# Kernel optimization log

Measured on AMD Instinct MI355X. Metric: run time of the kernel, lower is better.

Reference implementation:

```python
import jax, jax.numpy as jnp
import numpy as np

HEADS = 8
PATCH = 3
EPS = 1e-6


def conv2d(x, w, b, padding=0, groups=1):
    out = jax.lax.conv_general_dilated(
        x, w, (1, 1), [(padding, padding), (padding, padding)],
        feature_group_count=groups,
        dimension_numbers=("NCHW", "OIHW", "NCHW"))
    return out + b[None, :, None, None]


def unfold(x, p):
    # F.unfold(x, p, padding=(p-1)//2, stride=1) -> [B, C*p*p, H*W]
    B, C, H, W = x.shape
    pad = (p - 1) // 2
    xp = jnp.pad(x, ((0, 0), (0, 0), (pad, pad), (pad, pad)))
    patches = jnp.stack(
        [xp[:, :, i:i + H, j:j + W] for i in range(p) for j in range(p)],
        axis=2)  # [B, C, p*p, H, W] -- channel-major like torch unfold
    return patches.reshape(B, C * p * p, H * W)


def linear_attn(q, k, v):
    # q,k: [B, h, N, Dk]; v: [B, h, N, Dv]; ReLU-feature linear attention
    kv = jnp.einsum("bhnd,bhne->bhde", k, v)          # [B,h,Dk,Dv]
    ksum = jnp.sum(k, axis=2)                          # [B,h,Dk]
    num = jnp.einsum("bhnd,bhde->bhne", q, kv)         # [B,h,N,Dv]
    den = jnp.einsum("bhnd,bhd->bhn", q, ksum)[..., None] + EPS
    return num / den


def attn_block(x, qkv_w, qkv_b, proj_w, proj_b):
    B, C, H, W = x.shape
    qkv = conv2d(x, qkv_w, qkv_b)                      # [B, 3C, H, W]
    q, k, v = jnp.split(qkv, 3, axis=1)
    q = jax.nn.relu(q)
    k = jax.nn.relu(k)
    qp = unfold(q, PATCH)                              # [B, C*p*p, HW]
    kp = unfold(k, PATCH)
    N = H * W
    qh = qp.reshape(B, HEADS, -1, N).transpose(0, 1, 3, 2)  # [B,h,N,Dk]
    kh = kp.reshape(B, HEADS, -1, N).transpose(0, 1, 3, 2)
    vh = v.reshape(B, HEADS, -1, N).transpose(0, 1, 3, 2)   # [B,h,N,Dv]
    o = linear_attn(qh, kh, vh)                        # [B,h,N,Dv]
    o = o.transpose(0, 1, 3, 2).reshape(B, C, H, W)
    return conv2d(o, proj_w, proj_b, padding=1)


def ffn_block(x, w1, b1, dw, db, w2, b2):
    C = x.shape[1]
    h = jax.nn.gelu(conv2d(x, w1, b1), approximate=False)
    h = jax.nn.gelu(conv2d(h, dw, db, padding=1, groups=C), approximate=False)
    return conv2d(h, w2, b2)


def setup_inputs() -> dict:
    key = jax.random.key(0)
    ks = jax.random.split(key, 12)
    C = 64
    B, H, W = 2, 256, 256
    s = 0.05
    return {
        "x": jax.random.normal(ks[0], (B, C, H, W), jnp.float32),
        "qkv_w": jax.random.normal(ks[1], (3 * C, C, 1, 1), jnp.float32) * s,
        "qkv_b": jax.random.normal(ks[2], (3 * C,), jnp.float32) * s,
        "proj_w": jax.random.normal(ks[3], (C, C, 3, 3), jnp.float32) * s,
        "proj_b": jax.random.normal(ks[4], (C,), jnp.float32) * s,
        "ffn1_w": jax.random.normal(ks[5], (C, C, 1, 1), jnp.float32) * s,
        "ffn1_b": jax.random.normal(ks[6], (C,), jnp.float32) * s,
        "dw_w": jax.random.normal(ks[7], (C, 1, 3, 3), jnp.float32) * s,
        "dw_b": jax.random.normal(ks[8], (C,), jnp.float32) * s,
        "ffn2_w": jax.random.normal(ks[9], (C, C, 1, 1), jnp.float32) * s,
        "ffn2_b": jax.random.normal(ks[10], (C,), jnp.float32) * s,
    }


def reference(x, qkv_w, qkv_b, proj_w, proj_b, ffn1_w, ffn1_b, dw_w, dw_b, ffn2_w, ffn2_b):
    x = x + attn_block(x, qkv_w, qkv_b, proj_w, proj_b)
    x = x + ffn_block(x, ffn1_w, ffn1_b, dw_w, dw_b, ffn2_w, ffn2_b)
    return x
```

## Files before the change

### kernel.cpp

```cpp
#include <hip/hip_runtime.h>
#include <hip/hip_bf16.h>

typedef __hip_bfloat16 bf16;
typedef __attribute__((ext_vector_type(8))) short short8;
typedef __attribute__((ext_vector_type(4))) short short4v;
typedef __attribute__((ext_vector_type(4))) float floatx4;

#define NPIX 65536

__device__ __forceinline__ float b2f(bf16 v) { return __bfloat162float(v); }
__device__ __forceinline__ bf16 f2b(float v) { return __float2bfloat16(v); }
__device__ __forceinline__ short f2bs(float v) { bf16 t = __float2bfloat16(v); return *(short*)&t; }
__device__ __forceinline__ float us2f(unsigned short u) {
  union { unsigned int i; float f; } t; t.i = ((unsigned int)u) << 16; return t.f;
}
__device__ __forceinline__ float gelu_f(float v) {
  return 0.5f * v * (1.f + erff(v * 0.7071067811865476f));
}

#define OFF_KV  50331648u
#define OFF_KS  50368512u
#define OFF_WP  50373120u

__global__ void k_zero(float* __restrict__ p, int n) {
  int i = blockIdx.x * 256 + threadIdx.x;
  if (i < n) p[i] = 0.f;
}

__global__ void k_pack(const float* __restrict__ pw, bf16* __restrict__ wpack) {
  int i = blockIdx.x * 256 + threadIdx.x;
  int p = i >> 12, rem = i & 4095;
  int co = rem >> 6, ci = rem & 63;
  wpack[i] = f2b(pw[(co * 64 + ci) * 9 + p]);
}

__device__ __forceinline__ void stage_f32(const float* __restrict__ src, bf16* tile) {
  int tid = threadIdx.x;
  int px = tid & 127, chalf = tid >> 7;
#pragma unroll
  for (int it = 0; it < 8; ++it) {
    int ci0 = it * 8 + chalf * 4;
    short4v w;
#pragma unroll
    for (int j = 0; j < 4; ++j) w[j] = f2bs(src[((size_t)(ci0 + j) << 16) + px]);
    *(short4v*)&tile[px * 72 + ci0] = w;
  }
}

__device__ __forceinline__ void stage_bf16(const bf16* __restrict__ src, bf16* tile) {
  int tid = threadIdx.x;
  int px = tid & 127, chalf = tid >> 7;
  const unsigned short* s = (const unsigned short*)src;
#pragma unroll
  for (int it = 0; it < 8; ++it) {
    int ci0 = it * 8 + chalf * 4;
    short4v w;
#pragma unroll
    for (int j = 0; j < 4; ++j) w[j] = (short)s[((size_t)(ci0 + j) << 16) + px];
    *(short4v*)&tile[px * 72 + ci0] = w;
  }
}

__global__ __launch_bounds__(256) void k_qkv_mfma(const float* __restrict__ x,
                                                  const float* __restrict__ qkv_w,
                                                  const float* __restrict__ qkv_b,
                                                  bf16* __restrict__ qkv) {
  __shared__ __align__(16) bf16 tile[128 * 72];
  int tid = threadIdx.x;
  int wv = tid >> 6, ln = tid & 63;
  int n0 = blockIdx.x << 7, b = blockIdx.y;
  stage_f32(x + ((size_t)b << 22) + n0, tile);

  int m = ln & 15, quad = ln >> 4;
  int co = wv * 16 + m;
  short8 afrag[3][2];
#pragma unroll
  for (int sec = 0; sec < 3; ++sec)
#pragma unroll
    for (int s = 0; s < 2; ++s) {
      short8 af;
#pragma unroll
      for (int j = 0; j < 8; ++j)
        af[j] = f2bs(qkv_w[sec * 4096 + co * 64 + s * 32 + quad * 8 + j]);
      afrag[sec][s] = af;
    }
  __syncthreads();

  floatx4 acc[3][8];
#pragma unroll
  for (int sec = 0; sec < 3; ++sec)
#pragma unroll
    for (int nt = 0; nt < 8; ++nt) acc[sec][nt] = (floatx4){0.f, 0.f, 0.f, 0.f};

#pragma unroll
  for (int s = 0; s < 2; ++s) {
    int base = m * 72 + s * 32 + quad * 8;
#pragma unroll
    for (int nt = 0; nt < 8; ++nt) {
      short8 bfrag = *(const short8*)&tile[base + nt * 16 * 72];
#pragma unroll
      for (int sec = 0; sec < 3; ++sec)
        acc[sec][nt] = __builtin_amdgcn_mfma_f32_16x16x32_bf16(afrag[sec][s], bfrag,
                                                               acc[sec][nt], 0, 0, 0);
    }
  }

  bf16* qb = qkv + ((size_t)(b * 192) << 16);
#pragma unroll
  for (int sec = 0; sec < 3; ++sec) {
    bool relu = (sec < 2);
#pragma unroll
    for (int r = 0; r < 4; ++r) {
      int co_r = wv * 16 + quad * 4 + r;
      float bias = qkv_b[sec * 64 + co_r];
      bf16* op = qb + ((size_t)(sec * 64 + co_r) << 16) + n0;
#pragma unroll
      for (int nt = 0; nt < 8; ++nt) {
        float v = acc[sec][nt][r] + bias;
        if (relu) v = fmaxf(v, 0.f);
        op[nt * 16 + m] = f2b(v);
      }
    }
  }
}

__global__ __launch_bounds__(256) void k_ffn1_mfma(const float* __restrict__ xin,
                                                   const float* __restrict__ w1,
                                                   const float* __restrict__ b1,
                                                   bf16* __restrict__ qkv) {
  __shared__ __align__(16) bf16 tile[128 * 72];
  int tid = threadIdx.x;
  int wv = tid >> 6, ln = tid & 63;
  int n0 = blockIdx.x << 7, b = blockIdx.z;
  stage_f32(xin + ((size_t)b << 22) + n0, tile);

  int m = ln & 15, quad = ln >> 4;
  int co = wv * 16 + m;
  short8 afrag[2];
#pragma unroll
  for (int s = 0; s < 2; ++s) {
    short8 af;
#pragma unroll
    for (int j = 0; j < 8; ++j) af[j] = f2bs(w1[co * 64 + s * 32 + quad * 8 + j]);
    afrag[s] = af;
  }
  __syncthreads();

  floatx4 acc[8];
#pragma unroll
  for (int nt = 0; nt < 8; ++nt) acc[nt] = (floatx4){0.f, 0.f, 0.f, 0.f};
#pragma unroll
  for (int s = 0; s < 2; ++s) {
    int base = m * 72 + s * 32 + quad * 8;
#pragma unroll
    for (int nt = 0; nt < 8; ++nt) {
      short8 bfrag = *(const short8*)&tile[base + nt * 16 * 72];
      acc[nt] = __builtin_amdgcn_mfma_f32_16x16x32_bf16(afrag[s], bfrag, acc[nt], 0, 0, 0);
    }
  }

  bf16* qb = qkv + ((size_t)(b * 192) << 16);
#pragma unroll
  for (int r = 0; r < 4; ++r) {
    int co_r = wv * 16 + quad * 4 + r;
    float bias = b1[co_r];
    bf16* op = qb + ((size_t)co_r << 16) + n0;
#pragma unroll
    for (int nt = 0; nt < 8; ++nt)
      op[nt * 16 + m] = f2b(gelu_f(acc[nt][r] + bias));
  }
}

__global__ __launch_bounds__(256) void k_ffn2_mfma(const bf16* __restrict__ qkv,
                                                   const float* __restrict__ w2,
                                                   const float* __restrict__ b2,
                                                   float* __restrict__ out) {
  __shared__ __align__(16) bf16 tile[128 * 72];
  int tid = threadIdx.x;
  int wv = tid >> 6, ln = tid & 63;
  int n0 = blockIdx.x << 7, b = blockIdx.z;
  const bf16* qb = qkv + ((size_t)(b * 192) << 16);
  stage_bf16(qb + ((size_t)64 << 16) + n0, tile);

  int m = ln & 15, quad = ln >> 4;
  int co = wv * 16 + m;
  short8 afrag[2];
#pragma unroll
  for (int s = 0; s < 2; ++s) {
    short8 af;
#pragma unroll
    for (int j = 0; j < 8; ++j) af[j] = f2bs(w2[co * 64 + s * 32 + quad * 8 + j]);
    afrag[s] = af;
  }
  __syncthreads();

  floatx4 acc[8];
#pragma unroll
  for (int nt = 0; nt < 8; ++nt) acc[nt] = (floatx4){0.f, 0.f, 0.f, 0.f};
#pragma unroll
  for (int s = 0; s < 2; ++s) {
    int base = m * 72 + s * 32 + quad * 8;
#pragma unroll
    for (int nt = 0; nt < 8; ++nt) {
      short8 bfrag = *(const short8*)&tile[base + nt * 16 * 72];
      acc[nt] = __builtin_amdgcn_mfma_f32_16x16x32_bf16(afrag[s], bfrag, acc[nt], 0, 0, 0);
    }
  }

#pragma unroll
  for (int r = 0; r < 4; ++r) {
    int co_r = wv * 16 + quad * 4 + r;
    float bias = b2[co_r];
    float* op = out + ((size_t)b << 22) + ((size_t)co_r << 16) + n0;
#pragma unroll
    for (int nt = 0; nt < 8; ++nt) {
      int i = nt * 16 + m;
      op[i] = op[i] + bias + acc[nt][r];
    }
  }
}

template <int CTRL>
__device__ __forceinline__ float dpp_add(float v) {
  int t = __builtin_amdgcn_update_dpp(0, __builtin_bit_cast(int, v), CTRL, 0xf, 0xf, true);
  return v + __builtin_bit_cast(float, t);
}

__device__ __forceinline__ float rowsum16(float v) {
  v = dpp_add<0xB1>(v);
  v = dpp_add<0x4E>(v);
  v = dpp_add<0x141>(v);
  v = dpp_add<0x140>(v);
  return v;
}

__device__ __forceinline__ void loadrow10(const unsigned short* __restrict__ plane,
                                          int y, int x0, float kf[10]) {
  if ((unsigned)y < 256u) {
    const unsigned short* row = plane + y * 256;
    short8 k8 = *(const short8*)&row[x0];
#pragma unroll
    for (int j = 0; j < 8; ++j) kf[1 + j] = us2f((unsigned short)k8[j]);
    kf[0] = (x0 > 0) ? us2f(row[x0 - 1]) : 0.f;
    kf[9] = (x0 + 8 < 256) ? us2f(row[x0 + 8]) : 0.f;
  } else {
#pragma unroll
    for (int j = 0; j < 10; ++j) kf[j] = 0.f;
  }
}

__device__ __forceinline__ void loadrow6(const unsigned short* __restrict__ plane,
                                         int y, int x0, float kf[6]) {
  if ((unsigned)y < 256u) {
    const unsigned short* row = plane + y * 256;
    short4v k4 = *(const short4v*)&row[x0];
#pragma unroll
    for (int j = 0; j < 4; ++j) kf[1 + j] = us2f((unsigned short)k4[j]);
    kf[0] = (x0 > 0) ? us2f(row[x0 - 1]) : 0.f;
    kf[5] = (x0 + 4 < 256) ? us2f(row[x0 + 4]) : 0.f;
  } else {
#pragma unroll
    for (int j = 0; j < 6; ++j) kf[j] = 0.f;
  }
}

__global__ __launch_bounds__(256) void k_stats(const bf16* __restrict__ qkv,
                                               float* __restrict__ kv,
                                               float* __restrict__ ksum) {
  int tid = threadIdx.x;
  int chunk = blockIdx.x, c = blockIdx.y;
  int hz = blockIdx.z, h = hz & 7, b = hz >> 3;
  int r = tid >> 5, xseg = tid & 31;
  int y = (chunk << 3) + r;
  int x0 = xseg << 3;
  const bf16* qb = qkv + ((size_t)(b * 192) << 16);
  const unsigned short* kp = (const unsigned short*)qb + (((size_t)(64 + h * 8 + c)) << 16);
  const unsigned short* vp = (const unsigned short*)qb + (((size_t)(128 + h * 8)) << 16);

  float kf[3][10];
#pragma unroll
  for (int rr = 0; rr < 3; ++rr) loadrow10(kp, y + rr - 1, x0, kf[rr]);

  short8 varr[8];
#pragma unroll
  for (int e = 0; e < 8; ++e)
    varr[e] = *(const short8*)&vp[((size_t)e << 16) + y * 256 + x0];

  __shared__ float red[16][81];
  int r16 = tid >> 4;
  bool wr = (tid & 15) == 0;

#pragma unroll
  for (int rr = 0; rr < 3; ++rr)
#pragma unroll
    for (int t = 0; t < 3; ++t) {
      float s = 0.f;
#pragma unroll
      for (int i = 0; i < 8; ++i) s += kf[rr][i + t];
      s = rowsum16(s);
      if (wr) red[r16][72 + rr * 3 + t] = s;
    }

#pragma unroll
  for (int e = 0; e < 8; ++e) {
    float vf[8];
#pragma unroll
    for (int i = 0; i < 8; ++i) vf[i] = us2f((unsigned short)varr[e][i]);
#pragma unroll
    for (int rr = 0; rr < 3; ++rr)
#pragma unroll
      for (int t = 0; t < 3; ++t) {
        float s = 0.f;
#pragma unroll
        for (int i = 0; i < 8; ++i) s = fmaf(kf[rr][i + t], vf[i], s);
        s = rowsum16(s);
        if (wr) red[r16][(rr * 3 + t) * 8 + e] = s;
      }
  }
  __syncthreads();
  if (tid < 81) {
    float s = 0.f;
#pragma unroll
    for (int j = 0; j < 16; ++j) s += red[j][tid];
    int dbase = (b * 8 + h) * 72 + c * 9;
    if (tid < 72) atomicAdd(&kv[((dbase + (tid >> 3)) << 3) + (tid & 7)], s);
    else atomicAdd(&ksum[dbase + (tid - 72)], s);
  }
}

__global__ __launch_bounds__(256) void k_apply(bf16* __restrict__ qkv,
                                               const float* __restrict__ kv,
                                               const float* __restrict__ ksum) {
  int tid = threadIdx.x;
  int chunk = blockIdx.x, h = blockIdx.y, b = blockIdx.z;
  const float* kvb = kv + (size_t)((b * 8 + h) * 72) * 8;
  const float* ksb = ksum + (b * 8 + h) * 72;
  bf16* qb = qkv + ((size_t)(b * 192) << 16);
  bf16* opx = qb + ((size_t)128 << 16);

  __shared__ float skv[576];
  __shared__ float sks[72];
  for (int i = tid; i < 648; i += 256) {
    if (i < 576) skv[i] = kvb[i];
    else sks[i - 576] = ksb[i - 576];
  }
  __syncthreads();

  int r = tid >> 6, xseg = tid & 63;
  int y = (chunk << 2) + r;
  int x0 = xseg << 2;

  float num[8][4], den[4];
#pragma unroll
  for (int i = 0; i < 4; ++i) {
    den[i] = 0.f;
#pragma unroll
    for (int e = 0; e < 8; ++e) num[e][i] = 0.f;
  }

#pragma unroll 1
  for (int c = 0; c < 8; ++c) {
    const unsigned short* qp = (const unsigned short*)qb + ((size_t)(h * 8 + c) << 16);
    float kf[3][6];
#pragma unroll
    for (int rr = 0; rr < 3; ++rr) loadrow6(qp, y + rr - 1, x0, kf[rr]);
#pragma unroll
    for (int rr = 0; rr < 3; ++rr)
#pragma unroll
      for (int t = 0; t < 3; ++t) {
        int d = c * 9 + rr * 3 + t;
        float ksv = sks[d];
#pragma unroll
        for (int i = 0; i < 4; ++i) den[i] = fmaf(kf[rr][i + t], ksv, den[i]);
#pragma unroll
        for (int e = 0; e < 8; ++e) {
          float kvv = skv[d * 8 + e];
#pragma unroll
          for (int i = 0; i < 4; ++i) num[e][i] = fmaf(kf[rr][i + t], kvv, num[e][i]);
        }
      }
  }

#pragma unroll
  for (int i = 0; i < 4; ++i) {
    float inv = 1.f / (den[i] + 1e-6f);
    int n = y * 256 + x0 + i;
    short8 ov;
#pragma unroll
    for (int e = 0; e < 8; ++e) ov[e] = f2bs(num[e][i] * inv);
    *(short8*)&opx[((size_t)n << 6) + h * 8] = ov;
  }
}

__global__ __launch_bounds__(256) void k_proj_mfma(const bf16* __restrict__ qkv,
                                                   const bf16* __restrict__ wpack,
                                                   const float* __restrict__ proj_b,
                                                   const float* __restrict__ x,
                                                   float* __restrict__ out) {
  __shared__ __align__(16) bf16 tile[3 * 66 * 64];
  int tid = threadIdx.x;
  int wv = tid >> 6, ln = tid & 63;
  int quarter = blockIdx.x, y = blockIdx.y, b = blockIdx.z;
  const bf16* opx = qkv + ((size_t)(b * 192 + 128) << 16);
  int x0 = quarter << 6;
  int m = ln & 15, quad = ln >> 4;
  int co = wv * 16 + m;

  for (int q = tid; q < 1584; q += 256) {
    int slot = q >> 3, sub = q & 7;
    int dyr = slot / 66, px = slot - dyr * 66;
    int gy = y + dyr - 1, gx = x0 + px - 1;
    short8 val = {0, 0, 0, 0, 0, 0, 0, 0};
    if ((unsigned)gy < 256u && (unsigned)gx < 256u)
      val = *(const short8*)&opx[(((size_t)(gy << 8) + gx) << 6) + (sub << 3)];
    int ci0 = (sub ^ (px & 7)) << 3;
    *(short8*)&tile[(slot << 6) + ci0] = val;
  }
  __syncthreads();

  floatx4 acc[4];
#pragma unroll
  for (int nt = 0; nt < 4; ++nt) acc[nt] = (floatx4){0.f, 0.f, 0.f, 0.f};

#pragma unroll 1
  for (int dyr = 0; dyr < 3; ++dyr) {
    short8 af[6];
#pragma unroll
    for (int j = 0; j < 6; ++j) {
      int p = dyr * 3 + (j >> 1);
      int ci0 = (j & 1) * 32 + quad * 8;
      af[j] = *(const short8*)&wpack[(p * 64 + co) * 64 + ci0];
    }
    int slot0 = dyr * 66;
#pragma unroll
    for (int j = 0; j < 6; ++j) {
      int dx = j >> 1;
      int ci0 = (j & 1) * 32 + quad * 8;
#pragma unroll
      for (int nt = 0; nt < 4; ++nt) {
        int px = nt * 16 + m + dx;
        int ci = ci0 ^ ((px & 7) << 3);
        short8 bfrag = *(const short8*)&tile[((slot0 + px) << 6) + ci];
        acc[nt] = __builtin_amdgcn_mfma_f32_16x16x32_bf16(af[j], bfrag, acc[nt], 0, 0, 0);
      }
    }
  }

  float bias4[4];
#pragma unroll
  for (int r = 0; r < 4; ++r) bias4[r] = proj_b[wv * 16 + quad * 4 + r];
#pragma unroll
  for (int nt = 0; nt < 4; ++nt) {
    int gx = x0 + nt * 16 + m;
#pragma unroll
    for (int r = 0; r < 4; ++r) {
      int co_r = wv * 16 + quad * 4 + r;
      size_t idx = ((size_t)(b * 64 + co_r) << 16) + (y << 8) + gx;
      out[idx] = x[idx] + bias4[r] + acc[nt][r];
    }
  }
}

__global__ __launch_bounds__(256) void k_dw(bf16* __restrict__ qkv,
                                            const float* __restrict__ dw_w,
                                            const float* __restrict__ dw_b) {
  int blk = blockIdx.x;
  int b = blockIdx.z;
  int c = blk >> 5;
  int y0 = (blk & 31) << 3;
  int tid = threadIdx.x;
  int r = tid >> 5, xseg = tid & 31;
  int y = y0 + r, x0 = xseg << 3;
  bf16* qb = qkv + ((size_t)(b * 192) << 16);
  const unsigned short* ip = (const unsigned short*)qb + ((size_t)c << 16);

  float w[9];
#pragma unroll
  for (int p = 0; p < 9; ++p) w[p] = dw_w[c * 9 + p];
  float bias = dw_b[c];

  float kf[3][10];
#pragma unroll
  for (int rr = 0; rr < 3; ++rr) loadrow10(ip, y + rr - 1, x0, kf[rr]);

  short8 ov;
#pragma unroll
  for (int i = 0; i < 8; ++i) {
    float acc = bias;
#pragma unroll
    for (int rr = 0; rr < 3; ++rr)
#pragma unroll
      for (int t = 0; t < 3; ++t)
        acc = fmaf(kf[rr][i + t], w[rr * 3 + t], acc);
    ov[i] = f2bs(gelu_f(acc));
  }
  *(short8*)&qb[((size_t)(64 + c) << 16) + y * 256 + x0] = ov;
}

extern "C" void kernel_launch(void* const* d_in, const int* in_sizes, int n_in,
                              void* d_out, int out_size, void* d_ws, size_t ws_size,
                              hipStream_t stream) {
  const float* x      = (const float*)d_in[0];
  const float* qkv_w  = (const float*)d_in[1];
  const float* qkv_b  = (const float*)d_in[2];
  const float* proj_w = (const float*)d_in[3];
  const float* proj_b = (const float*)d_in[4];
  const float* ffn1_w = (const float*)d_in[5];
  const float* ffn1_b = (const float*)d_in[6];
  const float* dw_w   = (const float*)d_in[7];
  const float* dw_b   = (const float*)d_in[8];
  const float* ffn2_w = (const float*)d_in[9];
  const float* ffn2_b = (const float*)d_in[10];
  float* out = (float*)d_out;

  char* ws = (char*)d_ws;
  bf16*  qkvb  = (bf16*)ws;
  float* kvb   = (float*)(ws + OFF_KV);
  float* ksb   = (float*)(ws + OFF_KS);
  bf16*  wpack = (bf16*)(ws + OFF_WP);

  k_zero<<<41, 256, 0, stream>>>(kvb, 10368);
  k_pack<<<144, 256, 0, stream>>>(proj_w, wpack);

  k_qkv_mfma<<<dim3(512, 2), 256, 0, stream>>>(x, qkv_w, qkv_b, qkvb);
  k_stats<<<dim3(32, 8, 16), 256, 0, stream>>>(qkvb, kvb, ksb);
  k_apply<<<dim3(64, 8, 2), 256, 0, stream>>>(qkvb, kvb, ksb);
  k_proj_mfma<<<dim3(4, 256, 2), 256, 0, stream>>>(qkvb, wpack, proj_b, x, out);
  k_ffn1_mfma<<<dim3(512, 1, 2), 256, 0, stream>>>(out, ffn1_w, ffn1_b, qkvb);
  k_dw<<<dim3(2048, 1, 2), 256, 0, stream>>>(qkvb, dw_w, dw_b);
  k_ffn2_mfma<<<dim3(512, 1, 2), 256, 0, stream>>>(qkvb, ffn2_w, ffn2_b, out);
}
```

Measured before the change: 251.3 us.

## Fuse ffn1 pointwise conv into proj epilogue and merge zero-fill into pack

The proj kernel now writes its residual output into shared memory as bf16 and immediately applies the ffn1 1x1 conv with GELU via MFMA, writing the result to the workspace. This removes the separate ffn1 kernel and its re-read of the fp32 intermediate from global memory. The kv accumulator zeroing is folded into the weight-pack kernel to drop a launch. It adds extra syncs and register pressure to the proj kernel.

```diff
diff --git a/kernel.cpp b/kernel.cpp
--- a/kernel.cpp
+++ b/kernel.cpp
@@ -22,13 +22,10 @@
 #define OFF_KS  50368512u
 #define OFF_WP  50373120u
 
-__global__ void k_zero(float* __restrict__ p, int n) {
+__global__ void k_pack(const float* __restrict__ pw, bf16* __restrict__ wpack,
+                       float* __restrict__ kvz) {
   int i = blockIdx.x * 256 + threadIdx.x;
-  if (i < n) p[i] = 0.f;
-}
-
-__global__ void k_pack(const float* __restrict__ pw, bf16* __restrict__ wpack) {
-  int i = blockIdx.x * 256 + threadIdx.x;
+  if (i < 10368) kvz[i] = 0.f;
   int p = i >> 12, rem = i & 4095;
   int co = rem >> 6, ci = rem & 63;
   wpack[i] = f2b(pw[(co * 64 + ci) * 9 + p]);
@@ -121,53 +118,6 @@
         op[nt * 16 + m] = f2b(v);
       }
     }
-  }
-}
-
-__global__ __launch_bounds__(256) void k_ffn1_mfma(const float* __restrict__ xin,
-                                                   const float* __restrict__ w1,
-                                                   const float* __restrict__ b1,
-                                                   bf16* __restrict__ qkv) {
-  __shared__ __align__(16) bf16 tile[128 * 72];
-  int tid = threadIdx.x;
-  int wv = tid >> 6, ln = tid & 63;
-  int n0 = blockIdx.x << 7, b = blockIdx.z;
-  stage_f32(xin + ((size_t)b << 22) + n0, tile);
-
-  int m = ln & 15, quad = ln >> 4;
-  int co = wv * 16 + m;
-  short8 afrag[2];
-#pragma unroll
-  for (int s = 0; s < 2; ++s) {
-    short8 af;
-#pragma unroll
-    for (int j = 0; j < 8; ++j) af[j] = f2bs(w1[co * 64 + s * 32 + quad * 8 + j]);
-    afrag[s] = af;
-  }
-  __syncthreads();
-
-  floatx4 acc[8];
-#pragma unroll
-  for (int nt = 0; nt < 8; ++nt) acc[nt] = (floatx4){0.f, 0.f, 0.f, 0.f};
-#pragma unroll
-  for (int s = 0; s < 2; ++s) {
-    int base = m * 72 + s * 32 + quad * 8;
-#pragma unroll
-    for (int nt = 0; nt < 8; ++nt) {
-      short8 bfrag = *(const short8*)&tile[base + nt * 16 * 72];
-      acc[nt] = __builtin_amdgcn_mfma_f32_16x16x32_bf16(afrag[s], bfrag, acc[nt], 0, 0, 0);
-    }
-  }
-
-  bf16* qb = qkv + ((size_t)(b * 192) << 16);
-#pragma unroll
-  for (int r = 0; r < 4; ++r) {
-    int co_r = wv * 16 + quad * 4 + r;
-    float bias = b1[co_r];
-    bf16* op = qb + ((size_t)co_r << 16) + n0;
-#pragma unroll
-    for (int nt = 0; nt < 8; ++nt)
-      op[nt * 16 + m] = f2b(gelu_f(acc[nt][r] + bias));
   }
 }
 
@@ -392,10 +342,12 @@
   }
 }
 
-__global__ __launch_bounds__(256) void k_proj_mfma(const bf16* __restrict__ qkv,
+__global__ __launch_bounds__(256) void k_proj_ffn1(bf16* qkv,
                                                    const bf16* __restrict__ wpack,
                                                    const float* __restrict__ proj_b,
                                                    const float* __restrict__ x,
+                                                   const float* __restrict__ w1,
+                                                   const float* __restrict__ b1,
                                                    float* __restrict__ out) {
   __shared__ __align__(16) bf16 tile[3 * 66 * 64];
   int tid = threadIdx.x;
@@ -449,15 +401,59 @@
   float bias4[4];
 #pragma unroll
   for (int r = 0; r < 4; ++r) bias4[r] = proj_b[wv * 16 + quad * 4 + r];
+
+  __syncthreads();
+
+  int co0 = wv * 16 + quad * 4;
 #pragma unroll
   for (int nt = 0; nt < 4; ++nt) {
-    int gx = x0 + nt * 16 + m;
+    int px = nt * 16 + m;
+    int gx = x0 + px;
+    short4v v4;
 #pragma unroll
     for (int r = 0; r < 4; ++r) {
-      int co_r = wv * 16 + quad * 4 + r;
+      int co_r = co0 + r;
       size_t idx = ((size_t)(b * 64 + co_r) << 16) + (y << 8) + gx;
-      out[idx] = x[idx] + bias4[r] + acc[nt][r];
-    }
+      float ov = x[idx] + bias4[r] + acc[nt][r];
+      out[idx] = ov;
+      v4[r] = f2bs(ov);
+    }
+    int t2i = px * 64 + (((co0 >> 3) ^ (px & 7)) << 3) + (co0 & 7);
+    *(short4v*)&tile[t2i] = v4;
+  }
+  __syncthreads();
+
+  short8 af1[2];
+#pragma unroll
+  for (int s = 0; s < 2; ++s) {
+    short8 af;
+#pragma unroll
+    for (int j = 0; j < 8; ++j) af[j] = f2bs(w1[co * 64 + s * 32 + quad * 8 + j]);
+    af1[s] = af;
+  }
+  floatx4 acc1[4];
+#pragma unroll
+  for (int nt = 0; nt < 4; ++nt) acc1[nt] = (floatx4){0.f, 0.f, 0.f, 0.f};
+#pragma unroll
+  for (int s = 0; s < 2; ++s) {
+    int ci0 = s * 32 + quad * 8;
+#pragma unroll
+    for (int nt = 0; nt < 4; ++nt) {
+      int px = nt * 16 + m;
+      int ci = ci0 ^ ((px & 7) << 3);
+      short8 bfrag = *(const short8*)&tile[px * 64 + ci];
+      acc1[nt] = __builtin_amdgcn_mfma_f32_16x16x32_bf16(af1[s], bfrag, acc1[nt], 0, 0, 0);
+    }
+  }
+  bf16* qb = qkv + ((size_t)(b * 192) << 16);
+#pragma unroll
+  for (int r = 0; r < 4; ++r) {
+    int co_r = co0 + r;
+    float bias = b1[co_r];
+    bf16* op = qb + ((size_t)co_r << 16) + (y << 8) + x0;
+#pragma unroll
+    for (int nt = 0; nt < 4; ++nt)
+      op[nt * 16 + m] = f2b(gelu_f(acc1[nt][r] + bias));
   }
 }
 
@@ -519,14 +515,12 @@
   float* ksb   = (float*)(ws + OFF_KS);
   bf16*  wpack = (bf16*)(ws + OFF_WP);
 
-  k_zero<<<41, 256, 0, stream>>>(kvb, 10368);
-  k_pack<<<144, 256, 0, stream>>>(proj_w, wpack);
-
+  k_pack<<<144, 256, 0, stream>>>(proj_w, wpack, kvb);
   k_qkv_mfma<<<dim3(512, 2), 256, 0, stream>>>(x, qkv_w, qkv_b, qkvb);
   k_stats<<<dim3(32, 8, 16), 256, 0, stream>>>(qkvb, kvb, ksb);
   k_apply<<<dim3(64, 8, 2), 256, 0, stream>>>(qkvb, kvb, ksb);
-  k_proj_mfma<<<dim3(4, 256, 2), 256, 0, stream>>>(qkvb, wpack, proj_b, x, out);
-  k_ffn1_mfma<<<dim3(512, 1, 2), 256, 0, stream>>>(out, ffn1_w, ffn1_b, qkvb);
+  k_proj_ffn1<<<dim3(4, 256, 2), 256, 0, stream>>>(qkvb, wpack, proj_b, x,
+                                                   ffn1_w, ffn1_b, out);
   k_dw<<<dim3(2048, 1, 2), 256, 0, stream>>>(qkvb, dw_w, dw_b);
   k_ffn2_mfma<<<dim3(512, 1, 2), 256, 0, stream>>>(qkvb, ffn2_w, ffn2_b, out);
 }
```

Measured after the change: 243.5 us. -3.1%, faster.
